# Performance work log

Measured on AMD Instinct MI355X. Metric: run time of the kernel, lower is better.

## Reference

```python
import jax, jax.numpy as jnp
import numpy as np


def setup_inputs() -> dict:
    key = jax.random.key(0)
    k1, k2, k3 = jax.random.split(key, 3)
    B, S, D, H = 16, 4096, 512, 512
    inp = jax.random.normal(k1, (B, S, D), dtype=jnp.float32)
    # torch nn.Linear(D, 3*H): weight (3H, D), bias (3H,)
    W = jax.random.normal(k2, (3 * H, D), dtype=jnp.float32) * (1.0 / np.sqrt(D))
    b = jax.random.normal(k3, (3 * H,), dtype=jnp.float32) * 0.01
    return {"inp": inp, "W": W, "b": b}


def _forget_mult(z, f):
    # z, f: (B, S, H). h_t = f_t*z_t + (1-f_t)*h_{t-1}, h_{-1}=0 (hid=None)
    zt = jnp.swapaxes(z, 0, 1)  # (S, B, H)
    ft = jnp.swapaxes(f, 0, 1)
    h0 = jnp.zeros(z.shape[0:1] + z.shape[2:3], dtype=z.dtype)  # (B, H)

    def step(h, zf):
        zi, fi = zf
        h = fi * zi + (1.0 - fi) * h
        return h, h

    _, hs = jax.lax.scan(step, h0, (zt, ft))
    return jnp.swapaxes(hs, 0, 1)  # (B, S, H)


def reference(inp, W, b):
    # QRNNLayer forward: window=1, output_gate=True, batch_first=True,
    # backward=False, zoneout=0, hid=None.
    y = jnp.einsum('bsd,hd->bsh', inp, W) + b  # (B, S, 3H)
    z_gate, f_gate, o_gate = jnp.split(y, 3, axis=2)
    z_gate = jnp.tanh(z_gate)
    f_gate = jax.nn.sigmoid(f_gate)
    c_gate = _forget_mult(z_gate, f_gate)
    output = jax.nn.sigmoid(o_gate) * c_gate
    return output, c_gate[:, -1]
```

## Files before the change

### kernel.cpp

```cpp
#include <hip/hip_runtime.h>
#include <stdint.h>

#define Bdim 16
#define Sdim 4096
#define Hdim 512
#define Mdim (Bdim*Sdim)
#define N3   (3*Hdim)
#define Kdim 512
#define NCHUNK 64
#define CLEN  (Sdim/NCHUNK)

typedef __bf16 bf16;
typedef __bf16 bf16x4 __attribute__((ext_vector_type(4)));
typedef __bf16 bf16x8 __attribute__((ext_vector_type(8)));
typedef float  f32x4  __attribute__((ext_vector_type(4)));
typedef _Float16 f16;
typedef _Float16 f16x4 __attribute__((ext_vector_type(4)));
typedef _Float16 f16x8 __attribute__((ext_vector_type(8)));

__device__ __forceinline__ void gload_lds16(const void* g, void* l) {
  __builtin_amdgcn_global_load_lds(
      (const __attribute__((address_space(1))) uint32_t*)g,
      (__attribute__((address_space(3))) uint32_t*)l, 16, 0, 0);
}

__global__ void __launch_bounds__(256) cvt_kernel(const float4* __restrict__ in,
                                                  bf16x4* __restrict__ out, int n4) {
  int i = blockIdx.x * blockDim.x + threadIdx.x;
  if (i >= n4) return;
  float4 v = in[i];
  bf16x4 o;
  o.x = (bf16)v.x; o.y = (bf16)v.y; o.z = (bf16)v.z; o.w = (bf16)v.w;
  out[i] = o;
}

#define BM 256
#define BN 256
#define BK2 32
#define NT (Kdim/BK2)

__global__ void __launch_bounds__(512, 2) gemm_act_kernel(
    const bf16* __restrict__ A, const bf16* __restrict__ Wb,
    const float* __restrict__ bias,
    f16* __restrict__ zbuf, f16* __restrict__ fbuf, f16* __restrict__ ogbuf) {
  __shared__ char lds[65536];
  const int tid  = threadIdx.x;
  const int wid  = tid >> 6;
  const int lane = tid & 63;
  const int wr = wid >> 2, wc = wid & 3;
  const int bid = blockIdx.x;
  const int wg  = (bid & 7) * 192 + (bid >> 3);
  const int mt = wg / (N3 / BN);
  const int nt = wg % (N3 / BN);
  const int row0 = mt * BM;

  const bf16* Ag = A  + (size_t)row0 * Kdim;
  const bf16* Bg = Wb + (size_t)(nt * BN) * Kdim;

  uint32_t srcO[2];
  {
    int r_ = tid >> 2, slot = tid & 3;
    #pragma unroll
    for (int i = 0; i < 2; ++i) {
      int row = i * 128 + r_;
      srcO[i] = (uint32_t)(row * Kdim + ((slot ^ ((row >> 1) & 3)) << 3));
    }
  }
  const uint32_t dstBase = (uint32_t)(wid * 1024);

  uint32_t byteA[8], byteB[4];
  {
    int kslot = lane >> 4;
    #pragma unroll
    for (int m = 0; m < 8; ++m) {
      int row = wr * 128 + m * 16 + (lane & 15);
      byteA[m] = (uint32_t)(row * 64 + ((kslot ^ ((row >> 1) & 3)) << 4));
    }
    #pragma unroll
    for (int n = 0; n < 4; ++n) {
      int row = wc * 64 + n * 16 + (lane & 15);
      byteB[n] = (uint32_t)(16384 + row * 64 + ((kslot ^ ((row >> 1) & 3)) << 4));
    }
  }

  f32x4 acc[8][4];
  #pragma unroll
  for (int m = 0; m < 8; ++m)
    #pragma unroll
    for (int n = 0; n < 4; ++n)
      acc[m][n] = (f32x4){0.f, 0.f, 0.f, 0.f};

  {
    char* Ad = lds; char* Bd = lds + 16384;
    #pragma unroll
    for (int i = 0; i < 2; ++i) gload_lds16(Ag + srcO[i], Ad + i * 8192 + dstBase);
    #pragma unroll
    for (int i = 0; i < 2; ++i) gload_lds16(Bg + srcO[i], Bd + i * 8192 + dstBase);
  }
  __syncthreads();

  for (int t = 0; t < NT; ++t) {
    if (t + 1 < NT) {
      char* Ad = lds + ((t + 1) & 1) * 32768; char* Bd = Ad + 16384;
      #pragma unroll
      for (int i = 0; i < 2; ++i)
        gload_lds16(Ag + srcO[i] + (t + 1) * BK2, Ad + i * 8192 + dstBase);
      #pragma unroll
      for (int i = 0; i < 2; ++i)
        gload_lds16(Bg + srcO[i] + (t + 1) * BK2, Bd + i * 8192 + dstBase);
    }
    const char* Ab = lds + (t & 1) * 32768;
    bf16x8 af[8], bfrag[4];
    #pragma unroll
    for (int m = 0; m < 8; ++m) af[m] = *(const bf16x8*)(Ab + byteA[m]);
    #pragma unroll
    for (int n = 0; n < 4; ++n) bfrag[n] = *(const bf16x8*)(Ab + byteB[n]);
    __builtin_amdgcn_s_setprio(1);
    #pragma unroll
    for (int m = 0; m < 8; ++m)
      #pragma unroll
      for (int n = 0; n < 4; ++n)
        acc[m][n] = __builtin_amdgcn_mfma_f32_16x16x32_bf16(af[m], bfrag[n], acc[m][n], 0, 0, 0);
    __builtin_amdgcn_s_setprio(0);
    __syncthreads();
  }

  const int gate = nt >> 1;
  const int cbn  = (nt & 1) * 256;
  f16* dst = (gate == 0) ? zbuf : ((gate == 1) ? fbuf : ogbuf);
  float bv[4];
  #pragma unroll
  for (int n = 0; n < 4; ++n)
    bv[n] = bias[gate * Hdim + cbn + wc * 64 + n * 16 + (lane & 15)];

  #pragma unroll
  for (int R = 0; R < 2; ++R) {
    #pragma unroll
    for (int m4 = 0; m4 < 4; ++m4) {
      const int m = R * 4 + m4;
      #pragma unroll
      for (int n = 0; n < 4; ++n) {
        int col = wc * 64 + n * 16 + (lane & 15);
        #pragma unroll
        for (int r = 0; r < 4; ++r) {
          int Lrow = wr * 64 + m4 * 16 + (lane >> 4) * 4 + r;
          float y = acc[m][n][r] + bv[n];
          float v;
          if (gate == 0) {
            float e = __expf(2.f * y);
            v = 1.f - 2.f / (e + 1.f);
          } else {
            v = 1.f / (1.f + __expf(-y));
          }
          uint32_t byte = (uint32_t)(Lrow * 512 + col * 2) ^ ((uint32_t)(Lrow & 7) << 4);
          *(f16*)(lds + byte) = (f16)v;
        }
      }
    }
    __syncthreads();
    #pragma unroll
    for (int j = 0; j < 8; ++j) {
      int c = j * 512 + tid;
      int Lrow = c >> 5, col8 = c & 31;
      uint32_t byte = (uint32_t)(Lrow * 512 + col8 * 16) ^ ((uint32_t)(Lrow & 7) << 4);
      f16x8 v = *(const f16x8*)(lds + byte);
      int G = (Lrow >> 6) * 128 + R * 64 + (Lrow & 63);
      *(f16x8*)&dst[(size_t)(row0 + G) * Hdim + cbn + col8 * 8] = v;
    }
    __syncthreads();
  }
}

__global__ void __launch_bounds__(256) scanA_kernel(const f16x4* __restrict__ z4,
                                                    const f16x4* __restrict__ f4,
                                                    float* __restrict__ Pb,
                                                    float* __restrict__ Qb) {
  int u  = blockIdx.x * blockDim.x + threadIdx.x;
  int hq = u & 127;
  int bc = u >> 7;
  int b  = bc & (Bdim - 1);
  int c  = bc >> 4;
  size_t base = ((size_t)(b * Sdim + c * CLEN)) * 128 + hq;
  float P[4] = {1.f, 1.f, 1.f, 1.f}, Q[4] = {0.f, 0.f, 0.f, 0.f};
  #pragma unroll 4
  for (int s = 0; s < CLEN; ++s) {
    f16x4 fv = f4[base], zv = z4[base];
    #pragma unroll
    for (int j = 0; j < 4; ++j) {
      float f = (float)fv[j];
      Q[j] += f * ((float)zv[j] - Q[j]);
      P[j] *= (1.f - f);
    }
    base += 128;
  }
  int outi = ((c * Bdim + b) << 9) + hq * 4;
  *(float4*)&Pb[outi] = make_float4(P[0], P[1], P[2], P[3]);
  *(float4*)&Qb[outi] = make_float4(Q[0], Q[1], Q[2], Q[3]);
}

__global__ void __launch_bounds__(256) scanB_kernel(const float* __restrict__ Pb,
                                                    const float* __restrict__ Qb,
                                                    float* __restrict__ hin,
                                                    float* __restrict__ c_last) {
  int t = blockIdx.x * blockDim.x + threadIdx.x;
  int h = t & (Hdim - 1), b = t >> 9;
  float hs = 0.f;
  #pragma unroll 8
  for (int c = 0; c < NCHUNK; ++c) {
    hin[c * (Bdim * Hdim) + t] = hs;
    int u = ((c * Bdim + b) << 9) + h;
    hs = Pb[u] * hs + Qb[u];
  }
  c_last[t] = hs;
}

__global__ void __launch_bounds__(256) scanC_kernel(const f16x4* __restrict__ z4,
                                                    const f16x4* __restrict__ f4,
                                                    const f16x4* __restrict__ og4,
                                                    const float* __restrict__ hin,
                                                    float4* __restrict__ out4) {
  int u  = blockIdx.x * blockDim.x + threadIdx.x;
  int hq = u & 127;
  int bc = u >> 7;
  int b  = bc & (Bdim - 1);
  int c  = bc >> 4;
  float4 hv = *(const float4*)&hin[c * (Bdim * Hdim) + b * Hdim + hq * 4];
  float h[4] = {hv.x, hv.y, hv.z, hv.w};
  size_t base = ((size_t)(b * Sdim + c * CLEN)) * 128 + hq;
  #pragma unroll 4
  for (int s = 0; s < CLEN; ++s) {
    f16x4 fv = f4[base], zv = z4[base], ov = og4[base];
    float4 o;
    #pragma unroll
    for (int j = 0; j < 4; ++j) {
      h[j] += (float)fv[j] * ((float)zv[j] - h[j]);
    }
    o.x = (float)ov[0] * h[0]; o.y = (float)ov[1] * h[1];
    o.z = (float)ov[2] * h[2]; o.w = (float)ov[3] * h[3];
    out4[base] = o;
    base += 128;
  }
}

extern "C" void kernel_launch(void* const* d_in, const int* in_sizes, int n_in,
                              void* d_out, int out_size, void* d_ws, size_t ws_size,
                              hipStream_t stream) {
  const float* inp  = (const float*)d_in[0];
  const float* W    = (const float*)d_in[1];
  const float* bias = (const float*)d_in[2];
  float* out = (float*)d_out;

  char* ws = (char*)d_ws;
  bf16* Abf = (bf16*)(ws);
  bf16* Wbf = (bf16*)(ws + 67108864);
  f16*  zh  = (f16*) (ws + 68681728);
  f16*  fh  = (f16*) (ws + 135790592);
  f16*  ogh = (f16*) (ws + 202899456);
  float* Pb = (float*)(ws + 270008320);
  float* Qb = (float*)(ws + 272105472);
  float* hin= (float*)(ws + 274202624);

  {
    int n4 = (Mdim * Kdim) / 4;
    cvt_kernel<<<n4 / 256, 256, 0, stream>>>((const float4*)inp, (bf16x4*)Abf, n4);
  }
  {
    int n4 = (N3 * Kdim) / 4;
    cvt_kernel<<<n4 / 256, 256, 0, stream>>>((const float4*)W, (bf16x4*)Wbf, n4);
  }
  gemm_act_kernel<<<(Mdim / BM) * (N3 / BN), 512, 0, stream>>>(Abf, Wbf, bias,
                                                               zh, fh, ogh);
  scanA_kernel<<<(NCHUNK * Bdim * 128) / 256, 256, 0, stream>>>(
      (const f16x4*)zh, (const f16x4*)fh, Pb, Qb);
  scanB_kernel<<<(Bdim * Hdim) / 256, 256, 0, stream>>>(Pb, Qb, hin,
                                                        out + (size_t)Mdim * Hdim);
  scanC_kernel<<<(NCHUNK * Bdim * 128) / 256, 256, 0, stream>>>(
      (const f16x4*)zh, (const f16x4*)fh, (const f16x4*)ogh, hin, (float4*)out);
}
```

Baseline: 313.9 us.

## Fuse fp32-to-bf16 input conversion into GEMM tile loading

Drops the separate conversion kernel for the 64K x 512 fp32 input. The GEMM now streams fp32 A tiles straight into LDS with a new XOR swizzle and converts them to bf16 in registers before the MFMAs. This saves writing and re-reading a 64 MB bf16 copy, but each A tile moves twice as many global bytes. LDS grows to 96 KB per block, which may stop two blocks from sharing a CU, and the extra conversion instructions sit in the inner loop.

Result: slower. 385.3 us (+22.7%).

```diff
diff --git a/kernel.cpp b/kernel.cpp
--- a/kernel.cpp
+++ b/kernel.cpp
@@ -40,10 +40,10 @@
 #define NT (Kdim/BK2)
 
 __global__ void __launch_bounds__(512, 2) gemm_act_kernel(
-    const bf16* __restrict__ A, const bf16* __restrict__ Wb,
+    const float* __restrict__ A, const bf16* __restrict__ Wb,
     const float* __restrict__ bias,
     f16* __restrict__ zbuf, f16* __restrict__ fbuf, f16* __restrict__ ogbuf) {
-  __shared__ char lds[65536];
+  __shared__ char lds[98304];
   const int tid  = threadIdx.x;
   const int wid  = tid >> 6;
   const int lane = tid & 63;
@@ -54,33 +54,36 @@
   const int nt = wg % (N3 / BN);
   const int row0 = mt * BM;
 
-  const bf16* Ag = A  + (size_t)row0 * Kdim;
-  const bf16* Bg = Wb + (size_t)(nt * BN) * Kdim;
-
-  uint32_t srcO[2];
-  {
-    int r_ = tid >> 2, slot = tid & 3;
-    #pragma unroll
-    for (int i = 0; i < 2; ++i) {
-      int row = i * 128 + r_;
-      srcO[i] = (uint32_t)(row * Kdim + ((slot ^ ((row >> 1) & 3)) << 3));
-    }
+  const float* Ag = A  + (size_t)row0 * Kdim;
+  const bf16*  Bg = Wb + (size_t)(nt * BN) * Kdim;
+
+  uint32_t srcA[4];
+  #pragma unroll
+  for (int i = 0; i < 4; ++i) {
+    int c = i * 512 + tid;
+    int row = c >> 3, slot = c & 7;
+    srcA[i] = (uint32_t)(row * Kdim + ((slot ^ (row & 7)) << 2));
+  }
+  uint32_t srcB[2];
+  #pragma unroll
+  for (int i = 0; i < 2; ++i) {
+    int c = i * 512 + tid;
+    int row = c >> 2, slot = c & 3;
+    srcB[i] = (uint32_t)(row * Kdim + ((slot ^ ((row >> 1) & 3)) << 3));
   }
   const uint32_t dstBase = (uint32_t)(wid * 1024);
 
+  const int kslot = lane >> 4;
   uint32_t byteA[8], byteB[4];
-  {
-    int kslot = lane >> 4;
-    #pragma unroll
-    for (int m = 0; m < 8; ++m) {
-      int row = wr * 128 + m * 16 + (lane & 15);
-      byteA[m] = (uint32_t)(row * 64 + ((kslot ^ ((row >> 1) & 3)) << 4));
-    }
-    #pragma unroll
-    for (int n = 0; n < 4; ++n) {
-      int row = wc * 64 + n * 16 + (lane & 15);
-      byteB[n] = (uint32_t)(16384 + row * 64 + ((kslot ^ ((row >> 1) & 3)) << 4));
-    }
+  #pragma unroll
+  for (int m = 0; m < 8; ++m) {
+    int row = wr * 128 + m * 16 + (lane & 15);
+    byteA[m] = (uint32_t)(row * 128 + (((2 * kslot) ^ (row & 7)) << 4));
+  }
+  #pragma unroll
+  for (int n = 0; n < 4; ++n) {
+    int row = wc * 64 + n * 16 + (lane & 15);
+    byteB[n] = (uint32_t)(row * 64 + ((kslot ^ ((row >> 1) & 3)) << 4));
   }
 
   f32x4 acc[8][4];
@@ -91,30 +94,39 @@
       acc[m][n] = (f32x4){0.f, 0.f, 0.f, 0.f};
 
   {
-    char* Ad = lds; char* Bd = lds + 16384;
-    #pragma unroll
-    for (int i = 0; i < 2; ++i) gload_lds16(Ag + srcO[i], Ad + i * 8192 + dstBase);
-    #pragma unroll
-    for (int i = 0; i < 2; ++i) gload_lds16(Bg + srcO[i], Bd + i * 8192 + dstBase);
+    char* Ad = lds; char* Bd = lds + 65536;
+    #pragma unroll
+    for (int i = 0; i < 4; ++i) gload_lds16(Ag + srcA[i], Ad + i * 8192 + dstBase);
+    #pragma unroll
+    for (int i = 0; i < 2; ++i) gload_lds16(Bg + srcB[i], Bd + i * 8192 + dstBase);
   }
   __syncthreads();
 
   for (int t = 0; t < NT; ++t) {
     if (t + 1 < NT) {
-      char* Ad = lds + ((t + 1) & 1) * 32768; char* Bd = Ad + 16384;
+      char* Ad = lds + ((t + 1) & 1) * 32768;
+      char* Bd = lds + 65536 + ((t + 1) & 1) * 16384;
+      #pragma unroll
+      for (int i = 0; i < 4; ++i)
+        gload_lds16(Ag + srcA[i] + (t + 1) * BK2, Ad + i * 8192 + dstBase);
       #pragma unroll
       for (int i = 0; i < 2; ++i)
-        gload_lds16(Ag + srcO[i] + (t + 1) * BK2, Ad + i * 8192 + dstBase);
-      #pragma unroll
-      for (int i = 0; i < 2; ++i)
-        gload_lds16(Bg + srcO[i] + (t + 1) * BK2, Bd + i * 8192 + dstBase);
+        gload_lds16(Bg + srcB[i] + (t + 1) * BK2, Bd + i * 8192 + dstBase);
     }
     const char* Ab = lds + (t & 1) * 32768;
+    const char* Bb = lds + 65536 + (t & 1) * 16384;
     bf16x8 af[8], bfrag[4];
     #pragma unroll
-    for (int m = 0; m < 8; ++m) af[m] = *(const bf16x8*)(Ab + byteA[m]);
-    #pragma unroll
-    for (int n = 0; n < 4; ++n) bfrag[n] = *(const bf16x8*)(Ab + byteB[n]);
+    for (int m = 0; m < 8; ++m) {
+      float4 x = *(const float4*)(Ab + byteA[m]);
+      float4 y = *(const float4*)(Ab + (byteA[m] ^ 16u));
+      bf16x8 fr;
+      fr[0] = (bf16)x.x; fr[1] = (bf16)x.y; fr[2] = (bf16)x.z; fr[3] = (bf16)x.w;
+      fr[4] = (bf16)y.x; fr[5] = (bf16)y.y; fr[6] = (bf16)y.z; fr[7] = (bf16)y.w;
+      af[m] = fr;
+    }
+    #pragma unroll
+    for (int n = 0; n < 4; ++n) bfrag[n] = *(const bf16x8*)(Bb + byteB[n]);
     __builtin_amdgcn_s_setprio(1);
     #pragma unroll
     for (int m = 0; m < 8; ++m)
@@ -251,7 +263,6 @@
   float* out = (float*)d_out;
 
   char* ws = (char*)d_ws;
-  bf16* Abf = (bf16*)(ws);
   bf16* Wbf = (bf16*)(ws + 67108864);
   f16*  zh  = (f16*) (ws + 68681728);
   f16*  fh  = (f16*) (ws + 135790592);
@@ -261,14 +272,10 @@
   float* hin= (float*)(ws + 274202624);
 
   {
-    int n4 = (Mdim * Kdim) / 4;
-    cvt_kernel<<<n4 / 256, 256, 0, stream>>>((const float4*)inp, (bf16x4*)Abf, n4);
-  }
-  {
     int n4 = (N3 * Kdim) / 4;
     cvt_kernel<<<n4 / 256, 256, 0, stream>>>((const float4*)W, (bf16x4*)Wbf, n4);
   }
-  gemm_act_kernel<<<(Mdim / BM) * (N3 / BN), 512, 0, stream>>>(Abf, Wbf, bias,
+  gemm_act_kernel<<<(Mdim / BM) * (N3 / BN), 512, 0, stream>>>(inp, Wbf, bias,
                                                                zh, fh, ogh);
   scanA_kernel<<<(NCHUNK * Bdim * 128) / 256, 256, 0, stream>>>(
       (const f16x4*)zh, (const f16x4*)fh, Pb, Qb);
```

## Fuse fp32-to-bf16 input conversion into GEMM via register-staged tile loads

Applied to the files above, without the earlier changes.

Drops the separate conversion kernel that turned the fp32 activations into a bf16 copy. The GEMM now reads fp32 A tiles into registers, converts them to bf16 and writes them to LDS. Loads are software-pipelined two tiles ahead in place of the direct global-to-LDS loads, and the s_setprio hints are removed. This avoids a full read and write pass over the large input. In exchange the GEMM reads twice as many A bytes per tile, and the staging registers raise register pressure under 512-thread, 2-block launch bounds.

Result: slower. 379.6 us (+20.9%).

```diff
diff --git a/kernel.cpp b/kernel.cpp
--- a/kernel.cpp
+++ b/kernel.cpp
@@ -18,12 +18,6 @@
 typedef _Float16 f16x4 __attribute__((ext_vector_type(4)));
 typedef _Float16 f16x8 __attribute__((ext_vector_type(8)));
 
-__device__ __forceinline__ void gload_lds16(const void* g, void* l) {
-  __builtin_amdgcn_global_load_lds(
-      (const __attribute__((address_space(1))) uint32_t*)g,
-      (__attribute__((address_space(3))) uint32_t*)l, 16, 0, 0);
-}
-
 __global__ void __launch_bounds__(256) cvt_kernel(const float4* __restrict__ in,
                                                   bf16x4* __restrict__ out, int n4) {
   int i = blockIdx.x * blockDim.x + threadIdx.x;
@@ -40,7 +34,7 @@
 #define NT (Kdim/BK2)
 
 __global__ void __launch_bounds__(512, 2) gemm_act_kernel(
-    const bf16* __restrict__ A, const bf16* __restrict__ Wb,
+    const float* __restrict__ A, const bf16* __restrict__ Wb,
     const float* __restrict__ bias,
     f16* __restrict__ zbuf, f16* __restrict__ fbuf, f16* __restrict__ ogbuf) {
   __shared__ char lds[65536];
@@ -54,19 +48,19 @@
   const int nt = wg % (N3 / BN);
   const int row0 = mt * BM;
 
-  const bf16* Ag = A  + (size_t)row0 * Kdim;
-  const bf16* Bg = Wb + (size_t)(nt * BN) * Kdim;
-
-  uint32_t srcO[2];
+  const float* Ag = A  + (size_t)row0 * Kdim;
+  const bf16*  Bg = Wb + (size_t)(nt * BN) * Kdim;
+
+  uint32_t src[2];
   {
     int r_ = tid >> 2, slot = tid & 3;
     #pragma unroll
     for (int i = 0; i < 2; ++i) {
       int row = i * 128 + r_;
-      srcO[i] = (uint32_t)(row * Kdim + ((slot ^ ((row >> 1) & 3)) << 3));
-    }
-  }
-  const uint32_t dstBase = (uint32_t)(wid * 1024);
+      src[i] = (uint32_t)(row * Kdim + ((slot ^ ((row >> 1) & 3)) << 3));
+    }
+  }
+  const uint32_t dstB = (uint32_t)(tid * 16);
 
   uint32_t byteA[8], byteB[4];
   {
@@ -90,38 +84,55 @@
     for (int n = 0; n < 4; ++n)
       acc[m][n] = (f32x4){0.f, 0.f, 0.f, 0.f};
 
-  {
-    char* Ad = lds; char* Bd = lds + 16384;
-    #pragma unroll
-    for (int i = 0; i < 2; ++i) gload_lds16(Ag + srcO[i], Ad + i * 8192 + dstBase);
-    #pragma unroll
-    for (int i = 0; i < 2; ++i) gload_lds16(Bg + srcO[i], Bd + i * 8192 + dstBase);
-  }
+  float4 arg[2][2];
+  float4 brg[2];
+
+  #define LOADT(t_) do {                                                     \
+    const float* Ap = Ag + (t_) * BK2;                                       \
+    const bf16*  Bp = Bg + (t_) * BK2;                                       \
+    _Pragma("unroll")                                                        \
+    for (int i = 0; i < 2; ++i) {                                            \
+      arg[i][0] = *(const float4*)(Ap + src[i]);                             \
+      arg[i][1] = *(const float4*)(Ap + src[i] + 4);                         \
+      brg[i]    = *(const float4*)(const void*)(Bp + src[i]);                \
+    }                                                                        \
+  } while (0)
+
+  #define WRITET(t_) do {                                                    \
+    char* Ad = lds + ((t_) & 1) * 32768;                                     \
+    char* Bd = Ad + 16384;                                                   \
+    _Pragma("unroll")                                                        \
+    for (int i = 0; i < 2; ++i) {                                            \
+      bf16x8 fr;                                                             \
+      fr[0] = (bf16)arg[i][0].x; fr[1] = (bf16)arg[i][0].y;                  \
+      fr[2] = (bf16)arg[i][0].z; fr[3] = (bf16)arg[i][0].w;                  \
+      fr[4] = (bf16)arg[i][1].x; fr[5] = (bf16)arg[i][1].y;                  \
+      fr[6] = (bf16)arg[i][1].z; fr[7] = (bf16)arg[i][1].w;                  \
+      *(bf16x8*)(Ad + i * 8192 + dstB) = fr;                                 \
+      *(float4*)(Bd + i * 8192 + dstB) = brg[i];                             \
+    }                                                                        \
+  } while (0)
+
+  LOADT(0);
+  WRITET(0);
+  LOADT(1);
   __syncthreads();
 
+  #pragma unroll 2
   for (int t = 0; t < NT; ++t) {
-    if (t + 1 < NT) {
-      char* Ad = lds + ((t + 1) & 1) * 32768; char* Bd = Ad + 16384;
-      #pragma unroll
-      for (int i = 0; i < 2; ++i)
-        gload_lds16(Ag + srcO[i] + (t + 1) * BK2, Ad + i * 8192 + dstBase);
-      #pragma unroll
-      for (int i = 0; i < 2; ++i)
-        gload_lds16(Bg + srcO[i] + (t + 1) * BK2, Bd + i * 8192 + dstBase);
-    }
+    if (t + 1 < NT) WRITET(t + 1);
+    if (t + 2 < NT) LOADT(t + 2);
     const char* Ab = lds + (t & 1) * 32768;
     bf16x8 af[8], bfrag[4];
     #pragma unroll
     for (int m = 0; m < 8; ++m) af[m] = *(const bf16x8*)(Ab + byteA[m]);
     #pragma unroll
     for (int n = 0; n < 4; ++n) bfrag[n] = *(const bf16x8*)(Ab + byteB[n]);
-    __builtin_amdgcn_s_setprio(1);
     #pragma unroll
     for (int m = 0; m < 8; ++m)
       #pragma unroll
       for (int n = 0; n < 4; ++n)
         acc[m][n] = __builtin_amdgcn_mfma_f32_16x16x32_bf16(af[m], bfrag[n], acc[m][n], 0, 0, 0);
-    __builtin_amdgcn_s_setprio(0);
     __syncthreads();
   }
 
@@ -251,7 +262,6 @@
   float* out = (float*)d_out;
 
   char* ws = (char*)d_ws;
-  bf16* Abf = (bf16*)(ws);
   bf16* Wbf = (bf16*)(ws + 67108864);
   f16*  zh  = (f16*) (ws + 68681728);
   f16*  fh  = (f16*) (ws + 135790592);
@@ -261,14 +271,10 @@
   float* hin= (float*)(ws + 274202624);
 
   {
-    int n4 = (Mdim * Kdim) / 4;
-    cvt_kernel<<<n4 / 256, 256, 0, stream>>>((const float4*)inp, (bf16x4*)Abf, n4);
-  }
-  {
     int n4 = (N3 * Kdim) / 4;
     cvt_kernel<<<n4 / 256, 256, 0, stream>>>((const float4*)W, (bf16x4*)Wbf, n4);
   }
-  gemm_act_kernel<<<(Mdim / BM) * (N3 / BN), 512, 0, stream>>>(Abf, Wbf, bias,
+  gemm_act_kernel<<<(Mdim / BM) * (N3 / BN), 512, 0, stream>>>(inp, Wbf, bias,
                                                                zh, fh, ogh);
   scanA_kernel<<<(NCHUNK * Bdim * 128) / 256, 256, 0, stream>>>(
       (const f16x4*)zh, (const f16x4*)fh, Pb, Qb);
```
